# Performance work log

Hardware: AMD Instinct MI355X
Metric: run time of the kernel (lower is better)

## Reference

```python
import jax, jax.numpy as jnp
import numpy as np

B, D, C, N = 256, 512, 345, 50000
K = 5
ALPHA = 1.0
EPS = 1e-12


def setup_inputs() -> dict:
    key = jax.random.key(0)
    k1, k2, k3, k4, k5 = jax.random.split(key, 5)
    return {
        "features": jax.random.normal(k1, (B, D), dtype=jnp.float32),
        "predictions": jax.random.normal(k2, (B, C), dtype=jnp.float32),
        "fea_bank": jax.random.normal(k3, (N, D), dtype=jnp.float32),
        "score_bank": jax.random.uniform(k4, (N, C), dtype=jnp.float32, minval=1e-3, maxval=1.0),
        "trg_idx": jax.random.randint(k5, (B,), 0, N, dtype=jnp.int64),
    }


def reference(features, predictions, fea_bank, score_bank, trg_idx):
    softmax_out = jax.nn.softmax(predictions, axis=1)  # [B, C]

    # --- no_grad block: bank update + neighbor retrieval ---
    f_norm = features / jnp.maximum(
        jnp.linalg.norm(features, axis=1, keepdims=True), EPS
    )
    f_ng = jax.lax.stop_gradient(f_norm)
    s_ng = jax.lax.stop_gradient(softmax_out)
    fb = fea_bank.at[trg_idx].set(f_ng)       # [N, D]
    sb = score_bank.at[trg_idx].set(s_ng)     # [N, C]
    distance = f_ng @ fb.T                    # [B, N] cosine similarity
    _, idx_near = jax.lax.top_k(distance, K + 1)
    idx_near = idx_near[:, 1:]                # drop self -> [B, K]
    score_near = sb[idx_near]                 # [B, K, C]

    # F.kl_div(input=softmax_out (NOT log), target=score_near):
    # target * (log(target) - input), summed over C and K, mean over B.
    kl = score_near * (jnp.log(score_near) - softmax_out[:, None, :])
    loss = jnp.mean(kl.sum(-1).sum(-1))

    # dispersion: masked pairwise dot of softmax outputs (off-diagonal)
    dot = softmax_out @ softmax_out.T         # [B, B]
    mask = 1.0 - jnp.eye(B, dtype=dot.dtype)
    neg_pred = jnp.mean((dot * mask).sum(-1))
    loss = loss + ALPHA * neg_pred
    return loss
```

## Files before the change

kernel.cpp:

```cpp
#include <hip/hip_runtime.h>
#include <cstdint>

#define BB 256
#define DD 512
#define CC 345
#define NBANK 50000
#define NPAD 50048
#define KNEI 5
#define ALPHAC 1.0f
#define EPSN 1e-12f
#define NHALF 782
#define CSLOTS (NHALF * 2)

typedef short short8 __attribute__((ext_vector_type(8)));
typedef float f32x4 __attribute__((ext_vector_type(4)));
typedef unsigned long long u64;

__device__ inline uint32_t f2bf1(float x) {
    union { float f; uint32_t u; } v; v.f = x;
    return (v.u + 0x7FFFu + ((v.u >> 16) & 1u)) >> 16;
}
__device__ inline uint32_t pack2(float a, float b) {
    return f2bf1(a) | (f2bf1(b) << 16);
}
__device__ inline float bl(uint32_t x) {
    union { uint32_t u; float f; } v; v.u = x << 16; return v.f;
}
__device__ inline float bh(uint32_t x) {
    union { uint32_t u; float f; } v; v.u = x & 0xFFFF0000u; return v.f;
}
__device__ inline u64 mkkey(float v, int j) {
    union { float f; uint32_t u; } c; c.f = v;
    uint32_t b = c.u;
    uint32_t k = (b & 0x80000000u) ? ~b : (b | 0x80000000u);
    return ((u64)k << 32) | (uint32_t)(~j);
}
__device__ inline u64 umax64(u64 a, u64 b) { return a > b ? a : b; }
__device__ inline u64 shfl_xor_u64(u64 v, int m) {
    int lo = __shfl_xor((int)(uint32_t)v, m, 64);
    int hi = __shfl_xor((int)(v >> 32), m, 64);
    return ((u64)(uint32_t)hi << 32) | (uint32_t)lo;
}
__device__ inline void ins6u(u64 k, u64* lv) {
    if (k > lv[5]) {
        int q = 5;
        while (q > 0 && k > lv[q - 1]) { lv[q] = lv[q - 1]; q--; }
        lv[q] = k;
    }
}
__device__ inline void tree6u(u64* sv, int t, const u64* lv) {
#pragma unroll
    for (int r = 0; r < 6; r++) sv[t * 6 + r] = lv[r];
    __syncthreads();
    for (int s = 128; s > 0; s >>= 1) {
        if (t < s) {
            u64 av[6], bv[6], rv[6];
#pragma unroll
            for (int r = 0; r < 6; r++) { av[r] = sv[t * 6 + r]; bv[r] = sv[(t + s) * 6 + r]; }
            int x = 0, y = 0;
#pragma unroll
            for (int o = 0; o < 6; o++) {
                bool pk = av[x] > bv[y];
                rv[o] = pk ? av[x] : bv[y];
                x += pk; y += !pk;
            }
#pragma unroll
            for (int r = 0; r < 6; r++) sv[t * 6 + r] = rv[r];
        }
        __syncthreads();
    }
}
__device__ inline void async16(const void* g, void* l) {
    __builtin_amdgcn_global_load_lds(
        (const __attribute__((address_space(1))) unsigned int*)g,
        (__attribute__((address_space(3))) unsigned int*)l, 16, 0, 0);
}
__device__ inline size_t sw_off(int tile, int r, int ch) {
    return (size_t)tile * 8192 + r * 64 + ((ch ^ (r & 7)) * 8);
}

__global__ void repl_init_kernel(int* __restrict__ repl) {
    int idx = blockIdx.x * 256 + threadIdx.x;
    if (idx < NPAD) repl[idx] = -1;
}

__global__ void winner_kernel(const int* __restrict__ trg, int* __restrict__ repl,
                              float* __restrict__ out) {
    int t = threadIdx.x;
    __shared__ int st[BB];
    if (t == 0) out[0] = 0.f;
    st[t] = trg[t];
    __syncthreads();
    int mv = st[t];
    int w = 1;
    for (int b2 = t + 1; b2 < BB; b2++)
        if (st[b2] == mv) w = 0;
    if (w) repl[mv] = t;
}

__global__ void norm_softmax_kernel(const float* __restrict__ feat,
                                    const float* __restrict__ pred,
                                    unsigned short* __restrict__ fnb,
                                    unsigned short* __restrict__ fnb2,
                                    float* __restrict__ p) {
    int b = blockIdx.x, t = threadIdx.x;
    __shared__ float red[256];
    float x0 = feat[b * DD + t];
    float x1 = feat[b * DD + t + 256];
    red[t] = x0 * x0 + x1 * x1;
    __syncthreads();
    for (int s = 128; s > 0; s >>= 1) {
        if (t < s) red[t] += red[t + s];
        __syncthreads();
    }
    float inv = 1.0f / fmaxf(sqrtf(red[0]), EPSN);
    if (t < 64) {
        const f32x4* src = (const f32x4*)(feat + b * DD + t * 8);
        f32x4 f0 = src[0], f1 = src[1];
        uint4 u = make_uint4(pack2(f0[0] * inv, f0[1] * inv),
                             pack2(f0[2] * inv, f0[3] * inv),
                             pack2(f1[0] * inv, f1[1] * inv),
                             pack2(f1[2] * inv, f1[3] * inv));
        *(uint4*)(fnb + b * DD + t * 8) = u;
        int mtile = b >> 7, r = b & 127, kt = t >> 3, ch = t & 7;
        *(uint4*)(fnb2 + sw_off(mtile * 8 + kt, r, ch)) = u;
    }
    __syncthreads();
    float y0 = (t < CC) ? pred[b * CC + t] : -3.0e38f;
    float y1 = (t + 256 < CC) ? pred[b * CC + t + 256] : -3.0e38f;
    red[t] = fmaxf(y0, y1);
    __syncthreads();
    for (int s = 128; s > 0; s >>= 1) {
        if (t < s) red[t] = fmaxf(red[t], red[t + s]);
        __syncthreads();
    }
    float M = red[0];
    __syncthreads();
    float e0 = (t < CC) ? expf(y0 - M) : 0.f;
    float e1 = (t + 256 < CC) ? expf(y1 - M) : 0.f;
    red[t] = e0 + e1;
    __syncthreads();
    for (int s = 128; s > 0; s >>= 1) {
        if (t < s) red[t] += red[t + s];
        __syncthreads();
    }
    float si = 1.0f / red[0];
    if (t < CC) p[b * CC + t] = e0 * si;
    if (t + 256 < CC) p[b * CC + t + 256] = e1 * si;
}

__global__ __launch_bounds__(256) void gemm_topk_kernel(
        const unsigned short* __restrict__ fnb2, const float* __restrict__ bank,
        const unsigned short* __restrict__ fnb, const int* __restrict__ repl,
        u64* __restrict__ cand) {
    __shared__ __align__(16) char smem[24576];
    unsigned short* As = (unsigned short*)smem;
    unsigned short* Bs = (unsigned short*)(smem + 16384);

    int t = threadIdx.x;
    int bid = blockIdx.x;
    int ntb = bid >> 1;
    int rh  = bid & 1;
    int j0 = ntb * 64;
    int w = t >> 6, lane = t & 63, quad = lane >> 4, l16 = lane & 15;

    int br = t >> 2, cq = t & 3;
    int bj = j0 + br;
    int rp = (bj < NBANK) ? repl[bj] : -2;

    f32x4 acc[2][4];
#pragma unroll
    for (int mt = 0; mt < 2; mt++)
#pragma unroll
        for (int nt = 0; nt < 4; nt++)
            acc[mt][nt] = (f32x4){0.f, 0.f, 0.f, 0.f};

    const char* fnb2b = (const char*)fnb2;

    for (int kt = 0; kt < 8; kt++) {
        const char* asrc = fnb2b + (size_t)((rh * 8 + kt) * 16384 + w * 4096);
        char* adst = smem + w * 4096;
#pragma unroll
        for (int u = 0; u < 4; u++)
            async16(asrc + u * 1024 + lane * 16, adst + u * 1024);
        {
            uint4 b0, b1;
            if (rp >= 0) {
                const uint4* s = (const uint4*)(fnb + (size_t)rp * DD + kt * 64 + cq * 16);
                b0 = s[0]; b1 = s[1];
            } else if (rp == -1) {
                const f32x4* s = (const f32x4*)(bank + (size_t)bj * DD + kt * 64 + cq * 16);
                f32x4 f0 = s[0], f1 = s[1], f2 = s[2], f3 = s[3];
                b0 = make_uint4(pack2(f0[0], f0[1]), pack2(f0[2], f0[3]),
                                pack2(f1[0], f1[1]), pack2(f1[2], f1[3]));
                b1 = make_uint4(pack2(f2[0], f2[1]), pack2(f2[2], f2[3]),
                                pack2(f3[0], f3[1]), pack2(f3[2], f3[3]));
            } else {
                b0 = make_uint4(0, 0, 0, 0);
                b1 = make_uint4(0, 0, 0, 0);
            }
            int c0 = cq * 2;
            *(uint4*)(Bs + br * 64 + ((c0 ^ (br & 7)) * 8)) = b0;
            *(uint4*)(Bs + br * 64 + (((c0 + 1) ^ (br & 7)) * 8)) = b1;
        }
        __syncthreads();
#pragma unroll
        for (int ks = 0; ks < 2; ks++) {
            int swz = ((ks * 4 + quad) ^ (l16 & 7)) * 8;
            short8 af[2], bf[4];
#pragma unroll
            for (int mt = 0; mt < 2; mt++)
                af[mt] = *(const short8*)(As + (w * 32 + mt * 16 + l16) * 64 + swz);
#pragma unroll
            for (int nt = 0; nt < 4; nt++)
                bf[nt] = *(const short8*)(Bs + (nt * 16 + l16) * 64 + swz);
#pragma unroll
            for (int mt = 0; mt < 2; mt++)
#pragma unroll
                for (int nt = 0; nt < 4; nt++)
                    acc[mt][nt] = __builtin_amdgcn_mfma_f32_16x16x32_bf16(
                        af[mt], bf[nt], acc[mt][nt], 0, 0, 0);
        }
        __syncthreads();
    }

    bool maskPad[4];
#pragma unroll
    for (int nt = 0; nt < 4; nt++)
        maskPad[nt] = (ntb == NHALF - 1) && ((j0 + nt * 16 + l16) >= NBANK);

#pragma unroll
    for (int mt = 0; mt < 2; mt++)
#pragma unroll
        for (int r2 = 0; r2 < 4; r2++) {
            u64 k[4];
#pragma unroll
            for (int nt = 0; nt < 4; nt++) {
                int j = j0 + nt * 16 + l16;
                k[nt] = maskPad[nt] ? 0ull : mkkey(acc[mt][nt][r2], j);
            }
            u64 m = umax64(umax64(k[0], k[1]), umax64(k[2], k[3]));
#pragma unroll
            for (int off = 1; off < 16; off <<= 1)
                m = umax64(m, shfl_xor_u64(m, off));
            u64 top1 = m;
#pragma unroll
            for (int nt = 0; nt < 4; nt++) k[nt] = (k[nt] == top1) ? 0ull : k[nt];
            m = umax64(umax64(k[0], k[1]), umax64(k[2], k[3]));
#pragma unroll
            for (int off = 1; off < 16; off <<= 1)
                m = umax64(m, shfl_xor_u64(m, off));
            if (l16 == 0) {
                int gi = rh * 128 + w * 32 + mt * 16 + quad * 4 + r2;
                u64* cp = cand + (size_t)gi * CSLOTS + ntb * 2;
                cp[0] = top1; cp[1] = m;
            }
        }
}

__global__ __launch_bounds__(256) void merge_kernel(
        const u64* __restrict__ cand, const unsigned short* __restrict__ fnb,
        const float* __restrict__ bank, const int* __restrict__ repl,
        int* __restrict__ nidx) {
    int i = blockIdx.x, t = threadIdx.x;
    __shared__ u64 sv[1536];
    __shared__ uint32_t fm[25];
    __shared__ int fl[128];
    __shared__ int nf;
    __shared__ float a[512];
    const u64* cr = cand + (size_t)i * CSLOTS;

    u64 lv[6] = {0, 0, 0, 0, 0, 0};
    for (int q = t; q < CSLOTS; q += 256) ins6u(cr[q], lv);
    if (t < 25) fm[t] = 0;
    if (t == 0) nf = 0;
    tree6u(sv, t, lv);
    u64 M6 = sv[5];
    __syncthreads();
    for (int h = t; h < NHALF; h += 256) {
        if (cr[h * 2 + 1] >= M6) {
            int s = atomicAdd(&nf, 1);
            if (s < 128) fl[s] = h;
            atomicOr(&fm[h >> 5], 1u << (h & 31));
        }
    }
    __syncthreads();
    if (nf > 0) {
        uint32_t wrd = ((const uint32_t*)(fnb + (size_t)i * DD))[t];
        a[2 * t] = bl(wrd);
        a[2 * t + 1] = bh(wrd);
        __syncthreads();
        u64 l2[6] = {0, 0, 0, 0, 0, 0};
        for (int q = t; q < CSLOTS; q += 256) {
            int h = q >> 1;
            if (!((fm[h >> 5] >> (h & 31)) & 1u)) ins6u(cr[q], l2);
        }
        int nfl = nf < 128 ? nf : 128;
        for (int s = 0; s < nfl; s++) {
            int h = fl[s];
            if (t < 64) {
                int j = h * 64 + t;
                if (j < NBANK) {
                    int rp = repl[j];
                    float dot = 0.f;
                    if (rp >= 0) {
                        const uint32_t* rw = (const uint32_t*)(fnb + (size_t)rp * DD);
                        for (int kk = 0; kk < 256; kk++) {
                            uint32_t u = rw[kk];
                            dot += bl(u) * a[2 * kk] + bh(u) * a[2 * kk + 1];
                        }
                    } else {
                        const float* rw = bank + (size_t)j * DD;
                        for (int kk = 0; kk < DD; kk++)
                            dot += bl(f2bf1(rw[kk])) * a[kk];
                    }
                    ins6u(mkkey(dot, j), l2);
                }
            }
        }
        __syncthreads();
        tree6u(sv, t, l2);
    }
    if (t == 0) {
#pragma unroll
        for (int r = 1; r < 6; r++)
            nidx[i * KNEI + r - 1] = (int)(~(uint32_t)(sv[r] & 0xFFFFFFFFull));
    }
}

__global__ void kl_negpred_kernel(const float* __restrict__ p,
                                  const float* __restrict__ sbank,
                                  const int* __restrict__ nidx,
                                  const int* __restrict__ trg,
                                  float* __restrict__ out) {
    int bid = blockIdx.x, t = threadIdx.x;
    __shared__ float red[256];
    __shared__ float aux[256];
    if (bid < BB) {
        int b = bid;
        __shared__ int st[BB];
        __shared__ int sj[KNEI], sb[KNEI];
        st[t] = trg[t];
        __syncthreads();
        if (t < KNEI) {
            int j = nidx[b * KNEI + t];
            sj[t] = j;
            int src = -1;
            for (int b2 = 0; b2 < BB; b2++)
                if (st[b2] == j) src = b2;
            sb[t] = src;
        }
        __syncthreads();
        float local = 0.f;
        for (int k = 0; k < KNEI; k++) {
            int j = sj[k], src = sb[k];
            const float* srow = (src >= 0) ? (p + src * CC) : (sbank + (size_t)j * CC);
            for (int c = t; c < CC; c += 256) {
                float s = srow[c];
                local += s * (logf(s) - p[b * CC + c]);
            }
        }
        red[t] = local;
        __syncthreads();
        for (int s = 128; s > 0; s >>= 1) {
            if (t < s) red[t] += red[t + s];
            __syncthreads();
        }
        if (t == 0) atomicAdd(out, red[0] * (1.0f / BB));
    } else {
        int c = bid - BB;
        float v = p[t * CC + c];
        red[t] = v;
        aux[t] = v * v;
        __syncthreads();
        for (int s = 128; s > 0; s >>= 1) {
            if (t < s) { red[t] += red[t + s]; aux[t] += aux[t + s]; }
            __syncthreads();
        }
        if (t == 0) atomicAdd(out, ALPHAC * (red[0] * red[0] - aux[0]) * (1.0f / BB));
    }
}

extern "C" void kernel_launch(void* const* d_in, const int* in_sizes, int n_in,
                              void* d_out, int out_size, void* d_ws, size_t ws_size,
                              hipStream_t stream) {
    const float* feat  = (const float*)d_in[0];
    const float* pred  = (const float*)d_in[1];
    const float* bank  = (const float*)d_in[2];
    const float* sbank = (const float*)d_in[3];
    const int*   trg   = (const int*)d_in[4];
    float* out = (float*)d_out;

    char* ws = (char*)d_ws;
    unsigned short* fnb2 = (unsigned short*)ws;
    unsigned short* fnb  = (unsigned short*)(ws + 262144);
    float*          p    = (float*)(ws + 524288);
    int*            repl = (int*)(ws + 877568);
    u64*            cand = (u64*)(ws + 1077760);
    int*            nidx = (int*)(ws + 4280832);

    repl_init_kernel<<<(NPAD + 255) / 256, 256, 0, stream>>>(repl);
    winner_kernel<<<1, 256, 0, stream>>>(trg, repl, out);
    norm_softmax_kernel<<<BB, 256, 0, stream>>>(feat, pred, fnb, fnb2, p);
    gemm_topk_kernel<<<NHALF * 2, 256, 0, stream>>>(fnb2, bank, fnb, repl, cand);
    merge_kernel<<<BB, 256, 0, stream>>>(cand, fnb, bank, repl, nidx);
    kl_negpred_kernel<<<BB + CC, 256, 0, stream>>>(p, sbank, nidx, trg, out);
}
```

Before: 270.8 us.

## Software-pipeline bank GEMM loads and fuse init, merge and KL kernels

The GEMM/top-k kernel now double-buffers its A and B LDS tiles. It prefetches fp32 bank rows three k-steps ahead into registers and uses explicit vmcnt/lgkmcnt waits with a single barrier per step, so global loads overlap the MFMA work. The replacement-map init moves into the norm/softmax kernel, and the merge kernel is fused with the KL/dispersion kernel, which drops two launches and the nidx round trip. In exchange the kernel uses more registers and twice the LDS, and gains an occupancy hint of 3 blocks per CU, which may limit residency. The hand-written waitcnt counts are fragile.

```diff
diff --git a/kernel.cpp b/kernel.cpp
--- a/kernel.cpp
+++ b/kernel.cpp
@@ -79,31 +79,15 @@
     return (size_t)tile * 8192 + r * 64 + ((ch ^ (r & 7)) * 8);
 }
 
-__global__ void repl_init_kernel(int* __restrict__ repl) {
-    int idx = blockIdx.x * 256 + threadIdx.x;
-    if (idx < NPAD) repl[idx] = -1;
-}
-
-__global__ void winner_kernel(const int* __restrict__ trg, int* __restrict__ repl,
-                              float* __restrict__ out) {
-    int t = threadIdx.x;
-    __shared__ int st[BB];
-    if (t == 0) out[0] = 0.f;
-    st[t] = trg[t];
-    __syncthreads();
-    int mv = st[t];
-    int w = 1;
-    for (int b2 = t + 1; b2 < BB; b2++)
-        if (st[b2] == mv) w = 0;
-    if (w) repl[mv] = t;
-}
-
 __global__ void norm_softmax_kernel(const float* __restrict__ feat,
                                     const float* __restrict__ pred,
                                     unsigned short* __restrict__ fnb,
                                     unsigned short* __restrict__ fnb2,
-                                    float* __restrict__ p) {
+                                    float* __restrict__ p,
+                                    int* __restrict__ repl) {
     int b = blockIdx.x, t = threadIdx.x;
+    int gi = b * 256 + t;
+    if (gi < NPAD) repl[gi] = -1;
     __shared__ float red[256];
     float x0 = feat[b * DD + t];
     float x1 = feat[b * DD + t + 256];
@@ -149,13 +133,25 @@
     if (t + 256 < CC) p[b * CC + t + 256] = e1 * si;
 }
 
-__global__ __launch_bounds__(256) void gemm_topk_kernel(
+__global__ void winner_kernel(const int* __restrict__ trg, int* __restrict__ repl,
+                              float* __restrict__ out) {
+    int t = threadIdx.x;
+    __shared__ int st[BB];
+    if (t == 0) out[0] = 0.f;
+    st[t] = trg[t];
+    __syncthreads();
+    int mv = st[t];
+    int w = 1;
+    for (int b2 = t + 1; b2 < BB; b2++)
+        if (st[b2] == mv) w = 0;
+    if (w) repl[mv] = t;
+}
+
+__global__ __launch_bounds__(256, 3) void gemm_topk_kernel(
         const unsigned short* __restrict__ fnb2, const float* __restrict__ bank,
         const unsigned short* __restrict__ fnb, const int* __restrict__ repl,
         u64* __restrict__ cand) {
-    __shared__ __align__(16) char smem[24576];
-    unsigned short* As = (unsigned short*)smem;
-    unsigned short* Bs = (unsigned short*)(smem + 16384);
+    __shared__ __align__(16) char smem[49152];
 
     int t = threadIdx.x;
     int bid = blockIdx.x;
@@ -166,7 +162,17 @@
 
     int br = t >> 2, cq = t & 3;
     int bj = j0 + br;
-    int rp = (bj < NBANK) ? repl[bj] : -2;
+    int rpv = (j0 + lane < NBANK) ? repl[j0 + lane] : -2;
+    int hasP = __any(rpv >= 0);
+    int rp = __shfl(rpv, br);
+    int bjc = (bj < NBANK) ? bj : (NBANK - 1);
+
+    const char* fnb2b = (const char*)fnb2;
+    const f32x4* bsrc = (const f32x4*)(bank + (size_t)bjc * DD);
+    const uint4* psrc = (const uint4*)(fnb + (size_t)((rp >= 0) ? rp : 0) * DD);
+
+    f32x4 pf[3][4];
+    uint4 pu0, pu1;
 
     f32x4 acc[2][4];
 #pragma unroll
@@ -175,35 +181,65 @@
         for (int nt = 0; nt < 4; nt++)
             acc[mt][nt] = (f32x4){0.f, 0.f, 0.f, 0.f};
 
-    const char* fnb2b = (const char*)fnb2;
-
-    for (int kt = 0; kt < 8; kt++) {
-        const char* asrc = fnb2b + (size_t)((rh * 8 + kt) * 16384 + w * 4096);
+    {
+        const char* asrc = fnb2b + (size_t)(rh * 8 + 0) * 16384 + w * 4096;
         char* adst = smem + w * 4096;
 #pragma unroll
         for (int u = 0; u < 4; u++)
             async16(asrc + u * 1024 + lane * 16, adst + u * 1024);
-        {
-            uint4 b0, b1;
-            if (rp >= 0) {
-                const uint4* s = (const uint4*)(fnb + (size_t)rp * DD + kt * 64 + cq * 16);
-                b0 = s[0]; b1 = s[1];
-            } else if (rp == -1) {
-                const f32x4* s = (const f32x4*)(bank + (size_t)bj * DD + kt * 64 + cq * 16);
-                f32x4 f0 = s[0], f1 = s[1], f2 = s[2], f3 = s[3];
-                b0 = make_uint4(pack2(f0[0], f0[1]), pack2(f0[2], f0[3]),
-                                pack2(f1[0], f1[1]), pack2(f1[2], f1[3]));
-                b1 = make_uint4(pack2(f2[0], f2[1]), pack2(f2[2], f2[3]),
-                                pack2(f3[0], f3[1]), pack2(f3[2], f3[3]));
-            } else {
-                b0 = make_uint4(0, 0, 0, 0);
-                b1 = make_uint4(0, 0, 0, 0);
-            }
-            int c0 = cq * 2;
-            *(uint4*)(Bs + br * 64 + ((c0 ^ (br & 7)) * 8)) = b0;
-            *(uint4*)(Bs + br * 64 + (((c0 + 1) ^ (br & 7)) * 8)) = b1;
-        }
-        __syncthreads();
+    }
+    asm volatile("" ::: "memory");
+#pragma unroll
+    for (int s = 0; s < 3; s++)
+#pragma unroll
+        for (int i = 0; i < 4; i++)
+            pf[s][i] = bsrc[s * 16 + cq * 4 + i];
+    asm volatile("" ::: "memory");
+    if (hasP && rp >= 0) { pu0 = psrc[cq * 2]; pu1 = psrc[cq * 2 + 1]; }
+    asm volatile("" ::: "memory");
+    {
+        uint4 b0, b1;
+        if (rp >= 0)      { b0 = pu0; b1 = pu1; }
+        else if (rp == -1) {
+            b0 = make_uint4(pack2(pf[0][0][0], pf[0][0][1]), pack2(pf[0][0][2], pf[0][0][3]),
+                            pack2(pf[0][1][0], pf[0][1][1]), pack2(pf[0][1][2], pf[0][1][3]));
+            b1 = make_uint4(pack2(pf[0][2][0], pf[0][2][1]), pack2(pf[0][2][2], pf[0][2][3]),
+                            pack2(pf[0][3][0], pf[0][3][1]), pack2(pf[0][3][2], pf[0][3][3]));
+        } else { b0 = make_uint4(0, 0, 0, 0); b1 = make_uint4(0, 0, 0, 0); }
+        unsigned short* Bn = (unsigned short*)(smem + 32768);
+        int c0 = cq * 2;
+        *(uint4*)(Bn + br * 64 + ((c0 ^ (br & 7)) * 8)) = b0;
+        *(uint4*)(Bn + br * 64 + (((c0 + 1) ^ (br & 7)) * 8)) = b1;
+    }
+    asm volatile("s_waitcnt lgkmcnt(0)" ::: "memory");
+    asm volatile("s_waitcnt vmcnt(12)" ::: "memory");
+    __builtin_amdgcn_s_barrier();
+    asm volatile("" ::: "memory");
+
+#pragma unroll
+    for (int kt = 0; kt < 8; kt++) {
+        if (kt < 7) {
+            const char* asrc = fnb2b + (size_t)(rh * 8 + kt + 1) * 16384 + w * 4096;
+            char* adst = smem + ((kt + 1) & 1) * 16384 + w * 4096;
+#pragma unroll
+            for (int u = 0; u < 4; u++)
+                async16(asrc + u * 1024 + lane * 16, adst + u * 1024);
+        }
+        asm volatile("" ::: "memory");
+        if (kt + 3 < 8) {
+#pragma unroll
+            for (int i = 0; i < 4; i++)
+                pf[(kt + 3) % 3][i] = bsrc[(kt + 3) * 16 + cq * 4 + i];
+        }
+        asm volatile("" ::: "memory");
+        if (kt < 7 && hasP && rp >= 0) {
+            pu0 = psrc[(kt + 1) * 4 + cq * 2];
+            pu1 = psrc[(kt + 1) * 4 + cq * 2 + 1];
+        }
+        asm volatile("" ::: "memory");
+
+        const unsigned short* As = (const unsigned short*)(smem + (kt & 1) * 16384);
+        const unsigned short* Bs = (const unsigned short*)(smem + 32768 + (kt & 1) * 8192);
 #pragma unroll
         for (int ks = 0; ks < 2; ks++) {
             int swz = ((ks * 4 + quad) ^ (l16 & 7)) * 8;
@@ -221,7 +257,31 @@
                     acc[mt][nt] = __builtin_amdgcn_mfma_f32_16x16x32_bf16(
                         af[mt], bf[nt], acc[mt][nt], 0, 0, 0);
         }
-        __syncthreads();
+
+        if (kt < 7) {
+            uint4 b0, b1;
+            if (rp >= 0)      { b0 = pu0; b1 = pu1; }
+            else if (rp == -1) {
+                const f32x4* q = pf[(kt + 1) % 3];
+                b0 = make_uint4(pack2(q[0][0], q[0][1]), pack2(q[0][2], q[0][3]),
+                                pack2(q[1][0], q[1][1]), pack2(q[1][2], q[1][3]));
+                b1 = make_uint4(pack2(q[2][0], q[2][1]), pack2(q[2][2], q[2][3]),
+                                pack2(q[3][0], q[3][1]), pack2(q[3][2], q[3][3]));
+            } else { b0 = make_uint4(0, 0, 0, 0); b1 = make_uint4(0, 0, 0, 0); }
+            unsigned short* Bn = (unsigned short*)(smem + 32768 + ((kt + 1) & 1) * 8192);
+            int c0 = cq * 2;
+            *(uint4*)(Bn + br * 64 + ((c0 ^ (br & 7)) * 8)) = b0;
+            *(uint4*)(Bn + br * 64 + (((c0 + 1) ^ (br & 7)) * 8)) = b1;
+
+            asm volatile("s_waitcnt lgkmcnt(0)" ::: "memory");
+            if (kt <= 4) {
+                asm volatile("s_waitcnt vmcnt(4)" ::: "memory");
+            } else {
+                asm volatile("s_waitcnt vmcnt(0)" ::: "memory");
+            }
+            __builtin_amdgcn_s_barrier();
+            asm volatile("" ::: "memory");
+        }
     }
 
     bool maskPad[4];
@@ -258,11 +318,28 @@
         }
 }
 
-__global__ __launch_bounds__(256) void merge_kernel(
+__global__ __launch_bounds__(256) void mergekl_kernel(
         const u64* __restrict__ cand, const unsigned short* __restrict__ fnb,
         const float* __restrict__ bank, const int* __restrict__ repl,
-        int* __restrict__ nidx) {
-    int i = blockIdx.x, t = threadIdx.x;
+        const float* __restrict__ p, const float* __restrict__ sbank,
+        const int* __restrict__ trg, float* __restrict__ out) {
+    int bid = blockIdx.x, t = threadIdx.x;
+    __shared__ float red[256];
+    if (bid >= BB) {
+        __shared__ float aux[256];
+        int c = bid - BB;
+        float v = p[t * CC + c];
+        red[t] = v;
+        aux[t] = v * v;
+        __syncthreads();
+        for (int s = 128; s > 0; s >>= 1) {
+            if (t < s) { red[t] += red[t + s]; aux[t] += aux[t + s]; }
+            __syncthreads();
+        }
+        if (t == 0) atomicAdd(out, ALPHAC * (red[0] * red[0] - aux[0]) * (1.0f / BB));
+        return;
+    }
+    int i = bid;
     __shared__ u64 sv[1536];
     __shared__ uint32_t fm[25];
     __shared__ int fl[128];
@@ -321,64 +398,34 @@
         __syncthreads();
         tree6u(sv, t, l2);
     }
-    if (t == 0) {
-#pragma unroll
-        for (int r = 1; r < 6; r++)
-            nidx[i * KNEI + r - 1] = (int)(~(uint32_t)(sv[r] & 0xFFFFFFFFull));
-    }
-}
-
-__global__ void kl_negpred_kernel(const float* __restrict__ p,
-                                  const float* __restrict__ sbank,
-                                  const int* __restrict__ nidx,
-                                  const int* __restrict__ trg,
-                                  float* __restrict__ out) {
-    int bid = blockIdx.x, t = threadIdx.x;
-    __shared__ float red[256];
-    __shared__ float aux[256];
-    if (bid < BB) {
-        int b = bid;
-        __shared__ int st[BB];
-        __shared__ int sj[KNEI], sb[KNEI];
-        st[t] = trg[t];
-        __syncthreads();
-        if (t < KNEI) {
-            int j = nidx[b * KNEI + t];
-            sj[t] = j;
-            int src = -1;
-            for (int b2 = 0; b2 < BB; b2++)
-                if (st[b2] == j) src = b2;
-            sb[t] = src;
-        }
-        __syncthreads();
-        float local = 0.f;
-        for (int k = 0; k < KNEI; k++) {
-            int j = sj[k], src = sb[k];
-            const float* srow = (src >= 0) ? (p + src * CC) : (sbank + (size_t)j * CC);
-            for (int c = t; c < CC; c += 256) {
-                float s = srow[c];
-                local += s * (logf(s) - p[b * CC + c]);
-            }
-        }
-        red[t] = local;
-        __syncthreads();
-        for (int s = 128; s > 0; s >>= 1) {
-            if (t < s) red[t] += red[t + s];
-            __syncthreads();
-        }
-        if (t == 0) atomicAdd(out, red[0] * (1.0f / BB));
-    } else {
-        int c = bid - BB;
-        float v = p[t * CC + c];
-        red[t] = v;
-        aux[t] = v * v;
-        __syncthreads();
-        for (int s = 128; s > 0; s >>= 1) {
-            if (t < s) { red[t] += red[t + s]; aux[t] += aux[t + s]; }
-            __syncthreads();
-        }
-        if (t == 0) atomicAdd(out, ALPHAC * (red[0] * red[0] - aux[0]) * (1.0f / BB));
-    }
+    __shared__ int st[BB];
+    __shared__ int sj[KNEI], sb2[KNEI];
+    st[t] = trg[t];
+    if (t < KNEI) {
+        sj[t] = (int)(~(uint32_t)(sv[t + 1] & 0xFFFFFFFFull));
+        sb2[t] = -1;
+    }
+    __syncthreads();
+#pragma unroll
+    for (int k = 0; k < KNEI; k++)
+        if (st[t] == sj[k]) atomicMax(&sb2[k], t);
+    __syncthreads();
+    float local = 0.f;
+    for (int k = 0; k < KNEI; k++) {
+        int j = sj[k], src = sb2[k];
+        const float* srow = (src >= 0) ? (p + src * CC) : (sbank + (size_t)j * CC);
+        for (int c = t; c < CC; c += 256) {
+            float s = srow[c];
+            local += s * (logf(s) - p[i * CC + c]);
+        }
+    }
+    red[t] = local;
+    __syncthreads();
+    for (int s = 128; s > 0; s >>= 1) {
+        if (t < s) red[t] += red[t + s];
+        __syncthreads();
+    }
+    if (t == 0) atomicAdd(out, red[0] * (1.0f / BB));
 }
 
 extern "C" void kernel_launch(void* const* d_in, const int* in_sizes, int n_in,
@@ -397,12 +444,9 @@
     float*          p    = (float*)(ws + 524288);
     int*            repl = (int*)(ws + 877568);
     u64*            cand = (u64*)(ws + 1077760);
-    int*            nidx = (int*)(ws + 4280832);
-
-    repl_init_kernel<<<(NPAD + 255) / 256, 256, 0, stream>>>(repl);
+
+    norm_softmax_kernel<<<BB, 256, 0, stream>>>(feat, pred, fnb, fnb2, p, repl);
     winner_kernel<<<1, 256, 0, stream>>>(trg, repl, out);
-    norm_softmax_kernel<<<BB, 256, 0, stream>>>(feat, pred, fnb, fnb2, p);
     gemm_topk_kernel<<<NHALF * 2, 256, 0, stream>>>(fnb2, bank, fnb, repl, cand);
-    merge_kernel<<<BB, 256, 0, stream>>>(cand, fnb, bank, repl, nidx);
-    kl_negpred_kernel<<<BB + CC, 256, 0, stream>>>(p, sbank, nidx, trg, out);
-}
+    mergekl_kernel<<<BB + CC, 256, 0, stream>>>(cand, fnb, bank, repl, p, sbank, trg, out);
+}
```

After: 270.5 us. No clear change (-0.1%).

## Drop global replacement table, compute per-tile in shared memory and fuse merge with KL

Applied to the files above, without the earlier changes.

Removes the repl_init and winner kernels. Each GEMM block now builds its own 64-entry replacement map in shared memory from trg_idx using atomicMax, so the last duplicate still wins. The merge kernel is fused with the KL/dispersion kernel, and the out zeroing moves into the softmax kernel. This cuts the launch count from six to three and removes global traffic for the repl and nidx arrays. In exchange, each fallback candidate in the merge does a linear scan over trg.

```diff
diff --git a/kernel.cpp b/kernel.cpp
--- a/kernel.cpp
+++ b/kernel.cpp
@@ -5,7 +5,6 @@
 #define DD 512
 #define CC 345
 #define NBANK 50000
-#define NPAD 50048
 #define KNEI 5
 #define ALPHAC 1.0f
 #define EPSN 1e-12f
@@ -79,31 +78,14 @@
     return (size_t)tile * 8192 + r * 64 + ((ch ^ (r & 7)) * 8);
 }
 
-__global__ void repl_init_kernel(int* __restrict__ repl) {
-    int idx = blockIdx.x * 256 + threadIdx.x;
-    if (idx < NPAD) repl[idx] = -1;
-}
-
-__global__ void winner_kernel(const int* __restrict__ trg, int* __restrict__ repl,
-                              float* __restrict__ out) {
-    int t = threadIdx.x;
-    __shared__ int st[BB];
-    if (t == 0) out[0] = 0.f;
-    st[t] = trg[t];
-    __syncthreads();
-    int mv = st[t];
-    int w = 1;
-    for (int b2 = t + 1; b2 < BB; b2++)
-        if (st[b2] == mv) w = 0;
-    if (w) repl[mv] = t;
-}
-
 __global__ void norm_softmax_kernel(const float* __restrict__ feat,
                                     const float* __restrict__ pred,
                                     unsigned short* __restrict__ fnb,
                                     unsigned short* __restrict__ fnb2,
-                                    float* __restrict__ p) {
+                                    float* __restrict__ p,
+                                    float* __restrict__ out) {
     int b = blockIdx.x, t = threadIdx.x;
+    if (b == 0 && t == 0) out[0] = 0.f;
     __shared__ float red[256];
     float x0 = feat[b * DD + t];
     float x1 = feat[b * DD + t + 256];
@@ -151,11 +133,12 @@
 
 __global__ __launch_bounds__(256) void gemm_topk_kernel(
         const unsigned short* __restrict__ fnb2, const float* __restrict__ bank,
-        const unsigned short* __restrict__ fnb, const int* __restrict__ repl,
+        const unsigned short* __restrict__ fnb, const int* __restrict__ trg,
         u64* __restrict__ cand) {
     __shared__ __align__(16) char smem[24576];
     unsigned short* As = (unsigned short*)smem;
     unsigned short* Bs = (unsigned short*)(smem + 16384);
+    __shared__ int rpl[64];
 
     int t = threadIdx.x;
     int bid = blockIdx.x;
@@ -164,9 +147,18 @@
     int j0 = ntb * 64;
     int w = t >> 6, lane = t & 63, quad = lane >> 4, l16 = lane & 15;
 
+    if (t < 64) rpl[t] = -1;
+    int tv = trg[t];
+    __syncthreads();
+    {
+        int d = tv - j0;
+        if (d >= 0 && d < 64) atomicMax(&rpl[d], t);
+    }
+    __syncthreads();
+
     int br = t >> 2, cq = t & 3;
     int bj = j0 + br;
-    int rp = (bj < NBANK) ? repl[bj] : -2;
+    int rp = (bj < NBANK) ? rpl[br] : -2;
 
     f32x4 acc[2][4];
 #pragma unroll
@@ -258,18 +250,37 @@
         }
 }
 
-__global__ __launch_bounds__(256) void merge_kernel(
+__global__ __launch_bounds__(256) void mergekl_kernel(
         const u64* __restrict__ cand, const unsigned short* __restrict__ fnb,
-        const float* __restrict__ bank, const int* __restrict__ repl,
-        int* __restrict__ nidx) {
-    int i = blockIdx.x, t = threadIdx.x;
+        const float* __restrict__ bank, const int* __restrict__ trg,
+        const float* __restrict__ p, const float* __restrict__ sbank,
+        float* __restrict__ out) {
+    int bid = blockIdx.x, t = threadIdx.x;
+    __shared__ float red[256];
+    if (bid >= BB) {
+        __shared__ float aux[256];
+        int c = bid - BB;
+        float v = p[t * CC + c];
+        red[t] = v;
+        aux[t] = v * v;
+        __syncthreads();
+        for (int s = 128; s > 0; s >>= 1) {
+            if (t < s) { red[t] += red[t + s]; aux[t] += aux[t + s]; }
+            __syncthreads();
+        }
+        if (t == 0) atomicAdd(out, ALPHAC * (red[0] * red[0] - aux[0]) * (1.0f / BB));
+        return;
+    }
+    int i = bid;
     __shared__ u64 sv[1536];
     __shared__ uint32_t fm[25];
     __shared__ int fl[128];
     __shared__ int nf;
     __shared__ float a[512];
+    __shared__ int st[BB];
     const u64* cr = cand + (size_t)i * CSLOTS;
 
+    st[t] = trg[t];
     u64 lv[6] = {0, 0, 0, 0, 0, 0};
     for (int q = t; q < CSLOTS; q += 256) ins6u(cr[q], lv);
     if (t < 25) fm[t] = 0;
@@ -301,7 +312,9 @@
             if (t < 64) {
                 int j = h * 64 + t;
                 if (j < NBANK) {
-                    int rp = repl[j];
+                    int rp = -1;
+                    for (int b2 = 0; b2 < BB; b2++)
+                        if (st[b2] == j) rp = b2;
                     float dot = 0.f;
                     if (rp >= 0) {
                         const uint32_t* rw = (const uint32_t*)(fnb + (size_t)rp * DD);
@@ -321,64 +334,32 @@
         __syncthreads();
         tree6u(sv, t, l2);
     }
-    if (t == 0) {
-#pragma unroll
-        for (int r = 1; r < 6; r++)
-            nidx[i * KNEI + r - 1] = (int)(~(uint32_t)(sv[r] & 0xFFFFFFFFull));
-    }
-}
-
-__global__ void kl_negpred_kernel(const float* __restrict__ p,
-                                  const float* __restrict__ sbank,
-                                  const int* __restrict__ nidx,
-                                  const int* __restrict__ trg,
-                                  float* __restrict__ out) {
-    int bid = blockIdx.x, t = threadIdx.x;
-    __shared__ float red[256];
-    __shared__ float aux[256];
-    if (bid < BB) {
-        int b = bid;
-        __shared__ int st[BB];
-        __shared__ int sj[KNEI], sb[KNEI];
-        st[t] = trg[t];
-        __syncthreads();
-        if (t < KNEI) {
-            int j = nidx[b * KNEI + t];
-            sj[t] = j;
-            int src = -1;
-            for (int b2 = 0; b2 < BB; b2++)
-                if (st[b2] == j) src = b2;
-            sb[t] = src;
-        }
-        __syncthreads();
-        float local = 0.f;
-        for (int k = 0; k < KNEI; k++) {
-            int j = sj[k], src = sb[k];
-            const float* srow = (src >= 0) ? (p + src * CC) : (sbank + (size_t)j * CC);
-            for (int c = t; c < CC; c += 256) {
-                float s = srow[c];
-                local += s * (logf(s) - p[b * CC + c]);
-            }
-        }
-        red[t] = local;
-        __syncthreads();
-        for (int s = 128; s > 0; s >>= 1) {
-            if (t < s) red[t] += red[t + s];
-            __syncthreads();
-        }
-        if (t == 0) atomicAdd(out, red[0] * (1.0f / BB));
-    } else {
-        int c = bid - BB;
-        float v = p[t * CC + c];
-        red[t] = v;
-        aux[t] = v * v;
-        __syncthreads();
-        for (int s = 128; s > 0; s >>= 1) {
-            if (t < s) { red[t] += red[t + s]; aux[t] += aux[t + s]; }
-            __syncthreads();
-        }
-        if (t == 0) atomicAdd(out, ALPHAC * (red[0] * red[0] - aux[0]) * (1.0f / BB));
-    }
+    __shared__ int sj[KNEI], sb2[KNEI];
+    if (t < KNEI) {
+        sj[t] = (int)(~(uint32_t)(sv[t + 1] & 0xFFFFFFFFull));
+        sb2[t] = -1;
+    }
+    __syncthreads();
+#pragma unroll
+    for (int k = 0; k < KNEI; k++)
+        if (st[t] == sj[k]) atomicMax(&sb2[k], t);
+    __syncthreads();
+    float local = 0.f;
+    for (int k = 0; k < KNEI; k++) {
+        int j = sj[k], src = sb2[k];
+        const float* srow = (src >= 0) ? (p + src * CC) : (sbank + (size_t)j * CC);
+        for (int c = t; c < CC; c += 256) {
+            float s = srow[c];
+            local += s * (logf(s) - p[i * CC + c]);
+        }
+    }
+    red[t] = local;
+    __syncthreads();
+    for (int s = 128; s > 0; s >>= 1) {
+        if (t < s) red[t] += red[t + s];
+        __syncthreads();
+    }
+    if (t == 0) atomicAdd(out, red[0] * (1.0f / BB));
 }
 
 extern "C" void kernel_launch(void* const* d_in, const int* in_sizes, int n_in,
@@ -395,14 +376,9 @@
     unsigned short* fnb2 = (unsigned short*)ws;
     unsigned short* fnb  = (unsigned short*)(ws + 262144);
     float*          p    = (float*)(ws + 524288);
-    int*            repl = (int*)(ws + 877568);
-    u64*            cand = (u64*)(ws + 1077760);
-    int*            nidx = (int*)(ws + 4280832);
-
-    repl_init_kernel<<<(NPAD + 255) / 256, 256, 0, stream>>>(repl);
-    winner_kernel<<<1, 256, 0, stream>>>(trg, repl, out);
-    norm_softmax_kernel<<<BB, 256, 0, stream>>>(feat, pred, fnb, fnb2, p);
-    gemm_topk_kernel<<<NHALF * 2, 256, 0, stream>>>(fnb2, bank, fnb, repl, cand);
-    merge_kernel<<<BB, 256, 0, stream>>>(cand, fnb, bank, repl, nidx);
-    kl_negpred_kernel<<<BB + CC, 256, 0, stream>>>(p, sbank, nidx, trg, out);
-}
+    u64*            cand = (u64*)(ws + 877568);
+
+    norm_softmax_kernel<<<BB, 256, 0, stream>>>(feat, pred, fnb, fnb2, p, out);
+    gemm_topk_kernel<<<NHALF * 2, 256, 0, stream>>>(fnb2, bank, fnb, trg, cand);
+    mergekl_kernel<<<BB + CC, 256, 0, stream>>>(cand, fnb, bank, trg, p, sbank, out);
+}
```

New measurement: 264.0 us. -2.5%, faster.
